# Performance work log

Measured on AMD Instinct MI355X. Metric: run time of the kernel, lower is better.

## Reference

```python
import jax, jax.numpy as jnp
import numpy as np

B, N, D = 2, 2048, 1024          # batch, seq (= wh*ww), model dim
H, HD = 16, 64                   # heads, head_dim (inner_dim = H*HD = D)
MLP = 4096                       # SwiGLU hidden dim
WSY, WSX = 16, 32                # ws_y = wh//2, ws_x = ww//2  (wh=32, ww=64)
EPS = float(jnp.finfo(jnp.float32).eps)  # torch RMSNorm default eps


def setup_inputs() -> dict:
    key = jax.random.key(0)
    ks = jax.random.split(key, 8)
    return {
        "x": jax.random.normal(ks[0], (B, N, D), jnp.float32),
        "t": jax.random.normal(ks[1], (B,), jnp.float32),
        "dt": jax.random.normal(ks[2], (B, D), jnp.float32),
        "w_qkv": (jax.random.normal(ks[3], (3 * H * HD, D), jnp.float32) * 0.02),
        "w_o": (jax.random.normal(ks[4], (D, H * HD), jnp.float32) * 0.02),
        "w1": (jax.random.normal(ks[5], (2 * MLP, D), jnp.float32) * 0.02),
        "w2": (jax.random.normal(ks[6], (D, MLP), jnp.float32) * 0.02),
        "g_attn": jnp.ones((D,), jnp.float32),  # RMSNorm weight (attn)
        "g_ff": jnp.ones((D,), jnp.float32),    # RMSNorm weight (ffn)
    }


def _rms(x, g):
    return x * jax.lax.rsqrt(jnp.mean(x * x, axis=-1, keepdims=True) + EPS) * g


def _win(x):
    # 'b h (wc_y wc_x ws_y ws_x) d' -> 'b h (wc_y ws_y wc_x ws_x) d'
    b, h, n, d = x.shape
    return x.reshape(b, h, 2, 2, WSY, WSX, d).transpose(0, 1, 2, 4, 3, 5, 6).reshape(b, h, n, d)


def _unwin(x):
    # inverse of _win
    b, h, n, d = x.shape
    return x.reshape(b, h, 2, WSY, 2, WSX, d).transpose(0, 1, 2, 4, 3, 5, 6).reshape(b, h, n, d)


def reference(x, t, dt, w_qkv, w_o, w1, w2, g_attn, g_ff):
    # ---- SPAttention (pre-norm); all-to-all is identity on 1 device ----
    h = _rms(x, g_attn)
    qkv = h @ w_qkv.T                              # [B,N,3*H*HD]
    q, k, v = jnp.split(qkv, 3, axis=-1)
    as_heads = lambda z: z.reshape(B, N, H, HD).transpose(0, 2, 1, 3)  # b h n d
    q, k, v = _win(as_heads(q)), _win(as_heads(k)), _win(as_heads(v))
    # NOTE: the source computes RoPE2D(q), RoPE2D(k) but discards the result;
    # attention consumes the UNROTATED seq_gathered_q/k/v. Faithful: no rotation.
    scale = 1.0 / jnp.sqrt(jnp.float32(HD))        # SDPA default scale
    s = jnp.einsum('bhqd,bhkd->bhqk', q, k) * scale
    a = jax.nn.softmax(s, axis=-1)
    o = jnp.einsum('bhqk,bhkd->bhqd', a, v)
    o = _unwin(o).transpose(0, 2, 1, 3).reshape(B, N, H * HD)
    x = x + o @ w_o.T                               # residual
    # ---- SwiGLU FeedForward (pre-norm) + residual ----
    hf = _rms(x, g_ff)
    gate, up = jnp.split(hf @ w1.T, 2, axis=-1)
    return x + (jax.nn.silu(gate) * up) @ w2.T
```

## Files before the change

### kernel.cpp

```cpp
#include <hip/hip_runtime.h>
#include <cstdint>
#include <cstddef>

typedef __attribute__((ext_vector_type(8)))  __bf16 bf16x8;
typedef __attribute__((ext_vector_type(4)))  __bf16 bf16x4;
typedef __attribute__((ext_vector_type(4)))  float  f32x4;
typedef __attribute__((ext_vector_type(16))) float  f32x16;
typedef __attribute__((ext_vector_type(2)))  uint32_t u32x2;
typedef __attribute__((ext_vector_type(4)))  uint32_t u32x4;

#define MFMA_BF16(a, b, c) __builtin_amdgcn_mfma_f32_16x16x32_bf16((a), (b), (c), 0, 0, 0)
#define MFMA32(a, b, c)    __builtin_amdgcn_mfma_f32_32x32x16_bf16((a), (b), (c), 0, 0, 0)

__device__ __forceinline__ void gload_lds16(const __bf16* src, __bf16* lds_dst) {
    __builtin_amdgcn_global_load_lds(
        (const __attribute__((address_space(1))) void*)(const_cast<__bf16*>(src)),
        (__attribute__((address_space(3))) void*)(lds_dst), 16, 0, 0);
}

__device__ __forceinline__ uint32_t pack2(float a, float b) {
    uint16_t ua = __builtin_bit_cast(uint16_t, (__bf16)a);
    uint16_t ub = __builtin_bit_cast(uint16_t, (__bf16)b);
    return (uint32_t)ua | ((uint32_t)ub << 16);
}

__device__ __forceinline__ int xcd_swz(int lid, int n) {
    return (lid & 7) * (n >> 3) + (lid >> 3);
}

__global__ __launch_bounds__(256) void cvt4_kernel(const float* __restrict__ s0,
                                                   const float* __restrict__ s1,
                                                   const float* __restrict__ s2,
                                                   const float* __restrict__ s3,
                                                   __bf16* __restrict__ d0,
                                                   __bf16* __restrict__ d1,
                                                   __bf16* __restrict__ d2,
                                                   __bf16* __restrict__ d3) {
    int b = blockIdx.x;
    const float* s; __bf16* d; int off;
    if (b < 3072)       { s = s0; d = d0; off = b; }
    else if (b < 4096)  { s = s1; d = d1; off = b - 3072; }
    else if (b < 12288) { s = s2; d = d2; off = b - 4096; }
    else                { s = s3; d = d3; off = b - 12288; }
    int i = off * 256 + threadIdx.x;
    float4 v = reinterpret_cast<const float4*>(s)[i];
    bf16x4 o;
    o[0] = (__bf16)v.x; o[1] = (__bf16)v.y; o[2] = (__bf16)v.z; o[3] = (__bf16)v.w;
    reinterpret_cast<bf16x4*>(d)[i] = o;
}

__global__ __launch_bounds__(256) void rmsnorm_kernel(const float* __restrict__ x,
                                                      const float* __restrict__ g,
                                                      __bf16* __restrict__ out) {
    const int row = blockIdx.x;
    const int t = threadIdx.x;
    float4 v = reinterpret_cast<const float4*>(x + (size_t)row * 1024)[t];
    float ss = v.x * v.x + v.y * v.y + v.z * v.z + v.w * v.w;
#pragma unroll
    for (int m = 1; m < 64; m <<= 1) ss += __shfl_xor(ss, m);
    __shared__ float sred[4];
    if ((t & 63) == 0) sred[t >> 6] = ss;
    __syncthreads();
    float tot = sred[0] + sred[1] + sred[2] + sred[3];
    float rs = rsqrtf(tot * (1.0f / 1024.0f) + 1.1920928955078125e-07f);
    float4 gv = reinterpret_cast<const float4*>(g)[t];
    bf16x4 o;
    o[0] = (__bf16)(v.x * rs * gv.x);
    o[1] = (__bf16)(v.y * rs * gv.y);
    o[2] = (__bf16)(v.z * rs * gv.z);
    o[3] = (__bf16)(v.w * rs * gv.w);
    *reinterpret_cast<bf16x4*>(out + (size_t)row * 1024 + t * 4) = o;
}

__global__ __launch_bounds__(256) void rmsnorm_b_kernel(const __bf16* __restrict__ x,
                                                        const float* __restrict__ g,
                                                        __bf16* __restrict__ out) {
    const int row = blockIdx.x;
    const int t = threadIdx.x;
    bf16x4 v4 = reinterpret_cast<const bf16x4*>(x + (size_t)row * 1024)[t];
    float a = (float)v4[0], b = (float)v4[1], c = (float)v4[2], d = (float)v4[3];
    float ss = a * a + b * b + c * c + d * d;
#pragma unroll
    for (int m = 1; m < 64; m <<= 1) ss += __shfl_xor(ss, m);
    __shared__ float sred[4];
    if ((t & 63) == 0) sred[t >> 6] = ss;
    __syncthreads();
    float tot = sred[0] + sred[1] + sred[2] + sred[3];
    float rs = rsqrtf(tot * (1.0f / 1024.0f) + 1.1920928955078125e-07f);
    float4 gv = reinterpret_cast<const float4*>(g)[t];
    bf16x4 o;
    o[0] = (__bf16)(a * rs * gv.x);
    o[1] = (__bf16)(b * rs * gv.y);
    o[2] = (__bf16)(c * rs * gv.z);
    o[3] = (__bf16)(d * rs * gv.w);
    *reinterpret_cast<bf16x4*>(out + (size_t)row * 1024 + t * 4) = o;
}

template <int MODE, int NB, int SQ>
__global__ __launch_bounds__(256) void gemm_nt(const __bf16* __restrict__ A, int lda,
                                               const __bf16* __restrict__ B, int ldb,
                                               __bf16* __restrict__ outb,
                                               float* __restrict__ outf,
                                               const float* __restrict__ resid,
                                               const __bf16* __restrict__ residb,
                                               __bf16* __restrict__ vt,
                                               int K, int ldo) {
    constexpr int BN = NB * 32;
    __shared__ __attribute__((aligned(16))) __bf16 As[128 * 64];
    __shared__ __attribute__((aligned(16))) __bf16 Bs[BN * 64];
    const int t = threadIdx.x;
    const int lane = t & 63;
    const int wid = t >> 6;
    int bm, bn;
    if (SQ) {
        int lid = blockIdx.x + blockIdx.y * gridDim.x;
        int c = lid & 7, i = lid >> 3;
        bm = (c & 1) * 16 + (i & 15);
        bn = (c >> 1) * 16 + (i >> 4);
    } else {
        int nwg = gridDim.x * gridDim.y;
        int sid = xcd_swz(blockIdx.x + blockIdx.y * gridDim.x, nwg);
        bm = sid % gridDim.x; bn = sid / gridDim.x;
    }
    const int wm = (wid >> 1) * 64, wn = (wid & 1) * (NB * 16);
    f32x4 acc[4][NB] = {};

    for (int kt = 0; kt < K; kt += 64) {
        __syncthreads();
#pragma unroll
        for (int i = 0; i < 4; ++i) {
            int L = i * 256 + t;
            int r = L >> 3, s = L & 7;
            int c = s ^ (r & 7);
            gload_lds16(A + (size_t)(bm * 128 + r) * lda + kt + c * 8, As + L * 8);
        }
#pragma unroll
        for (int i = 0; i < NB; ++i) {
            int L = i * 256 + t;
            int r = L >> 3, s = L & 7;
            int c = s ^ (r & 7);
            int rb = bn * BN + r;
            int srow = (MODE == 2) ? ((rb >> 1) + ((rb & 1) << 12)) : rb;
            gload_lds16(B + (size_t)srow * ldb + kt + c * 8, Bs + L * 8);
        }
        __syncthreads();
#pragma unroll
        for (int ks = 0; ks < 2; ++ks) {
            bf16x8 af[4], bfr[NB];
#pragma unroll
            for (int mi = 0; mi < 4; ++mi) {
                int r = wm + mi * 16 + (lane & 15);
                int slot = (ks * 4 + (lane >> 4)) ^ (r & 7);
                af[mi] = *reinterpret_cast<const bf16x8*>(As + r * 64 + slot * 8);
            }
#pragma unroll
            for (int ni = 0; ni < NB; ++ni) {
                int r = wn + ni * 16 + (lane & 15);
                int slot = (ks * 4 + (lane >> 4)) ^ (r & 7);
                bfr[ni] = *reinterpret_cast<const bf16x8*>(Bs + r * 64 + slot * 8);
            }
            __builtin_amdgcn_s_setprio(1);
#pragma unroll
            for (int mi = 0; mi < 4; ++mi)
#pragma unroll
                for (int ni = 0; ni < NB; ++ni)
                    acc[mi][ni] = MFMA_BF16(af[mi], bfr[ni], acc[mi][ni]);
            __builtin_amdgcn_s_setprio(0);
        }
    }
    const int row0 = bm * 128 + wm + ((lane >> 4) << 2);
    const int col0 = bn * BN + wn + (lane & 15);
    if (MODE == 4 && bn >= 16) {
#pragma unroll
        for (int mi = 0; mi < 4; ++mi)
#pragma unroll
            for (int ni = 0; ni < NB; ++ni) {
                bf16x4 o4;
#pragma unroll
                for (int r2 = 0; r2 < 4; ++r2) o4[r2] = (__bf16)acc[mi][ni][r2];
                int n0 = row0 + mi * 16;
                int bb = n0 >> 11, nn = n0 & 2047;
                int vc = col0 + ni * 16 - 2048;
                *reinterpret_cast<bf16x4*>(
                    vt + ((size_t)(bb * 16 + (vc >> 6)) * 64 + (vc & 63)) * 2048 + nn) = o4;
            }
        return;
    }
#pragma unroll
    for (int mi = 0; mi < 4; ++mi)
#pragma unroll
        for (int ni = 0; ni < NB; ++ni)
#pragma unroll
            for (int r2 = 0; r2 < 4; ++r2) {
                int row = row0 + mi * 16 + r2;
                int col = col0 + ni * 16;
                float v = acc[mi][ni][r2];
                size_t idx = (size_t)row * ldo + col;
                if (MODE == 0 || MODE == 4) {
                    outb[idx] = (__bf16)v;
                } else if (MODE == 1) {
                    outb[idx] = (__bf16)(v + resid[idx]);
                } else if (MODE == 3) {
                    outf[idx] = v + (float)residb[idx];
                } else {
                    float pv = __shfl_xor(v, 1);
                    if (!(lane & 1)) {
                        float sg = v / (1.0f + __expf(-v));
                        outb[(size_t)row * ldo + (col >> 1)] = (__bf16)(sg * pv);
                    }
                }
            }
}

__global__ __launch_bounds__(256) void attn_kernel(const __bf16* __restrict__ qkv,
                                                   const __bf16* __restrict__ vt,
                                                   float* __restrict__ opart,
                                                   float* __restrict__ lpart) {
    __shared__ __attribute__((aligned(16))) __bf16 Ks[128 * 64];
    __shared__ __attribute__((aligned(16))) __bf16 Vs[64 * 128];
    const int t = threadIdx.x;
    const int lane = t & 63;
    const int w = t >> 6;
    const int hi = lane >> 5;
    const int l31 = lane & 31;
    const int nwg = gridDim.x * gridDim.y;
    const int sid = xcd_swz(blockIdx.x + blockIdx.y * gridDim.x, nwg);
    const int qb = sid % gridDim.x;
    const int bh = sid / gridDim.x;
    const int kz = blockIdx.z;
    const int b = bh >> 4, h = bh & 15;
    const __bf16* qp = qkv + (size_t)b * 2048 * 3072 + h * 64;
    const __bf16* kp = qp + 1024;
    const __bf16* vtp = vt + (size_t)bh * 64 * 2048;
    const int q0 = qb * 128 + w * 32;

    const float SC = 0.18033688011112042f;
    bf16x8 qf[4];
#pragma unroll
    for (int s = 0; s < 4; ++s) {
        bf16x8 raw = *reinterpret_cast<const bf16x8*>(
            qp + (size_t)(q0 + l31) * 3072 + s * 16 + hi * 8);
        bf16x8 sc;
#pragma unroll
        for (int j = 0; j < 8; ++j) sc[j] = (__bf16)((float)raw[j] * SC);
        qf[s] = sc;
    }

    f32x16 oa[2] = {};
    float l_run = 0.0f;

    auto stage = [&](int kt) {
#pragma unroll
        for (int i = 0; i < 4; ++i) {
            int L = i * 256 + t;
            int r = L >> 3, s = L & 7;
            int c = s ^ (r & 7);
            gload_lds16(kp + (size_t)(kt + r) * 3072 + c * 8, &Ks[L * 8]);
        }
#pragma unroll
        for (int i = 0; i < 4; ++i) {
            int L = i * 256 + t;
            int r = L >> 4, s = L & 15;
            int c = s ^ (r & 15);
            gload_lds16(vtp + (size_t)r * 2048 + kt + c * 8, &Vs[L * 8]);
        }
    };

    const int kt0 = kz * 1024;
    for (int kt = kt0; kt < kt0 + 1024; kt += 128) {
        stage(kt);
        asm volatile("s_waitcnt vmcnt(0)\n\ts_barrier" ::: "memory");

#pragma unroll
        for (int h2 = 0; h2 < 2; ++h2) {
            f32x16 st[2];
#pragma unroll
            for (int r = 0; r < 16; ++r) { st[0][r] = -6.0f; st[1][r] = -6.0f; }
            __builtin_amdgcn_s_setprio(1);
#pragma unroll
            for (int s = 0; s < 4; ++s) {
#pragma unroll
                for (int mb = 0; mb < 2; ++mb) {
                    int r = h2 * 64 + mb * 32 + l31;
                    int sl = (s * 2 + hi) ^ (r & 7);
                    bf16x8 kf = *reinterpret_cast<const bf16x8*>(&Ks[r * 64 + sl * 8]);
                    st[mb] = MFMA32(kf, qf[s], st[mb]);
                }
            }
            __builtin_amdgcn_s_setprio(0);

            float ps = 0.0f;
#pragma unroll
            for (int mb = 0; mb < 2; ++mb)
#pragma unroll
                for (int r = 0; r < 16; ++r) {
                    float p = exp2f(st[mb][r]);
                    st[mb][r] = p;
                    ps += p;
                }
            ps += __shfl_xor(ps, 32);
            l_run += ps;

            uint32_t pk[16];
#pragma unroll
            for (int mb = 0; mb < 2; ++mb)
#pragma unroll
                for (int i2 = 0; i2 < 8; ++i2)
                    pk[mb * 8 + i2] = pack2(st[mb][2 * i2], st[mb][2 * i2 + 1]);

            __builtin_amdgcn_s_setprio(1);
#pragma unroll
            for (int s2 = 0; s2 < 4; ++s2) {
                const int I0 = (s2 >> 1) * 8 + (s2 & 1) * 4;
                u32x2 w02 = __builtin_amdgcn_permlane32_swap(pk[I0], pk[I0 + 2], false, false);
                u32x2 w13 = __builtin_amdgcn_permlane32_swap(pk[I0 + 1], pk[I0 + 3], false, false);
                u32x4 fv;
                fv[0] = w02[0]; fv[1] = w13[0]; fv[2] = w02[1]; fv[3] = w13[1];
                bf16x8 pa = __builtin_bit_cast(bf16x8, fv);
#pragma unroll
                for (int nb = 0; nb < 2; ++nb) {
                    int rv = nb * 32 + l31;
                    int ch = h2 * 8 + s2 * 2 + hi;
                    int sl = ch ^ (rv & 15);
                    bf16x8 vf = *reinterpret_cast<const bf16x8*>(&Vs[rv * 128 + sl * 8]);
                    oa[nb] = MFMA32(pa, vf, oa[nb]);
                }
            }
            __builtin_amdgcn_s_setprio(0);
        }
        __syncthreads();
    }

#pragma unroll
    for (int r = 0; r < 16; ++r) {
        int crow = (r & 3) + 8 * (r >> 2) + 4 * hi;
        int row = q0 + crow;
        size_t base = (size_t)kz * 4194304 + ((size_t)b * 2048 + row) * 1024 + h * 64 + l31;
        opart[base]      = oa[0][r];
        opart[base + 32] = oa[1][r];
    }
    if (hi == 0)
        lpart[kz * 65536 + bh * 2048 + q0 + l31] = l_run;
}

__global__ __launch_bounds__(256) void attn_comb(const float* __restrict__ op,
                                                 const float* __restrict__ lp,
                                                 __bf16* __restrict__ o) {
    const int row = blockIdx.x;
    const int t = threadIdx.x;
    const int b = row >> 11, q = row & 2047;
    const int c0 = t * 4;
    const int h = c0 >> 6;
    const int li = (b * 16 + h) * 2048 + q;
    float l = lp[li] + lp[65536 + li];
    float inv = 1.0f / l;
    float4 p0 = *reinterpret_cast<const float4*>(op + (size_t)row * 1024 + c0);
    float4 p1 = *reinterpret_cast<const float4*>(op + 4194304 + (size_t)row * 1024 + c0);
    bf16x4 o4;
    o4[0] = (__bf16)((p0.x + p1.x) * inv);
    o4[1] = (__bf16)((p0.y + p1.y) * inv);
    o4[2] = (__bf16)((p0.z + p1.z) * inv);
    o4[3] = (__bf16)((p0.w + p1.w) * inv);
    *reinterpret_cast<bf16x4*>(o + (size_t)row * 1024 + c0) = o4;
}

extern "C" void kernel_launch(void* const* d_in, const int* in_sizes, int n_in,
                              void* d_out, int out_size, void* d_ws, size_t ws_size,
                              hipStream_t stream) {
    const float* x      = (const float*)d_in[0];
    const float* w_qkv  = (const float*)d_in[3];
    const float* w_o    = (const float*)d_in[4];
    const float* w1     = (const float*)d_in[5];
    const float* w2     = (const float*)d_in[6];
    const float* g_attn = (const float*)d_in[7];
    const float* g_ff   = (const float*)d_in[8];
    float* out = (float*)d_out;

    char* ws = (char*)d_ws;
    size_t off = 0;
    auto alloc = [&](size_t bytes) -> void* {
        void* p = ws + off;
        off += (bytes + 255) & ~(size_t)255;
        return p;
    };
    __bf16* wqkv_b = (__bf16*)alloc((size_t)3072 * 1024 * 2);
    __bf16* wo_b   = (__bf16*)alloc((size_t)1024 * 1024 * 2);
    __bf16* w1_b   = (__bf16*)alloc((size_t)8192 * 1024 * 2);
    __bf16* w2_b   = (__bf16*)alloc((size_t)1024 * 4096 * 2);
    __bf16* h_b    = (__bf16*)alloc((size_t)4096 * 1024 * 2);
    __bf16* qkv_b  = (__bf16*)alloc((size_t)4096 * 3072 * 2);
    __bf16* o_b    = (__bf16*)alloc((size_t)4096 * 1024 * 2);
    __bf16* x2b    = (__bf16*)alloc((size_t)4096 * 1024 * 2);
    __bf16* vt_b   = (__bf16*)alloc((size_t)32 * 64 * 2048 * 2);
    float*  opart  = (float*)alloc((size_t)2 * 4096 * 1024 * 4);
    float*  lpart  = (float*)alloc((size_t)2 * 32 * 2048 * 4);
    __bf16* act_b  = qkv_b;

    cvt4_kernel<<<16384, 256, 0, stream>>>(w_qkv, w_o, w1, w2,
                                           wqkv_b, wo_b, w1_b, w2_b);

    rmsnorm_kernel<<<4096, 256, 0, stream>>>(x, g_attn, h_b);
    gemm_nt<4, 4, 0><<<dim3(32, 24), 256, 0, stream>>>(h_b, 1024, wqkv_b, 1024,
                                                       qkv_b, nullptr, nullptr, nullptr,
                                                       vt_b, 1024, 3072);
    attn_kernel<<<dim3(16, 32, 2), 256, 0, stream>>>(qkv_b, vt_b, opart, lpart);
    attn_comb<<<4096, 256, 0, stream>>>(opart, lpart, o_b);
    gemm_nt<1, 2, 0><<<dim3(32, 16), 256, 0, stream>>>(o_b, 1024, wo_b, 1024,
                                                       x2b, nullptr, x, nullptr,
                                                       nullptr, 1024, 1024);
    rmsnorm_b_kernel<<<4096, 256, 0, stream>>>(x2b, g_ff, h_b);
    gemm_nt<2, 4, 1><<<dim3(32, 64), 256, 0, stream>>>(h_b, 1024, w1_b, 1024,
                                                       act_b, nullptr, nullptr, nullptr,
                                                       nullptr, 1024, 4096);
    gemm_nt<3, 2, 0><<<dim3(32, 16), 256, 0, stream>>>(act_b, 4096, w2_b, 4096,
                                                       nullptr, out, nullptr, x2b,
                                                       nullptr, 4096, 1024);
}
```

Before: 308.6 us.

## Switch GEMM inner loop to 32x32x16 MFMA with precomputed load offsets

Replaces the 16x16x32 bf16 MFMA tiles in the shared GEMM kernel with 32x32x16 MFMA, so each wave covers its tile with fewer, larger matrix instructions and fewer LDS fragment reads per FLOP. Global-load source pointers and swizzled LDS read offsets are now computed once before the K loop instead of on every iteration. The epilogues are rewritten for the 32x32 accumulator layout. This raises accumulator register pressure and changes the LDS access pattern, which could affect occupancy or bank conflicts.

Result: no change. 312.8 us (+1.4%).

```diff
diff --git a/kernel.cpp b/kernel.cpp
--- a/kernel.cpp
+++ b/kernel.cpp
@@ -9,8 +9,7 @@
 typedef __attribute__((ext_vector_type(2)))  uint32_t u32x2;
 typedef __attribute__((ext_vector_type(4)))  uint32_t u32x4;
 
-#define MFMA_BF16(a, b, c) __builtin_amdgcn_mfma_f32_16x16x32_bf16((a), (b), (c), 0, 0, 0)
-#define MFMA32(a, b, c)    __builtin_amdgcn_mfma_f32_32x32x16_bf16((a), (b), (c), 0, 0, 0)
+#define MFMA32(a, b, c) __builtin_amdgcn_mfma_f32_32x32x16_bf16((a), (b), (c), 0, 0, 0)
 
 __device__ __forceinline__ void gload_lds16(const __bf16* src, __bf16* lds_dst) {
     __builtin_amdgcn_global_load_lds(
@@ -96,7 +95,7 @@
     *reinterpret_cast<bf16x4*>(out + (size_t)row * 1024 + t * 4) = o;
 }
 
-template <int MODE, int NB, int SQ>
+template <int MODE, int BN32, int SQ>
 __global__ __launch_bounds__(256) void gemm_nt(const __bf16* __restrict__ A, int lda,
                                                const __bf16* __restrict__ B, int ldb,
                                                __bf16* __restrict__ outb,
@@ -105,12 +104,15 @@
                                                const __bf16* __restrict__ residb,
                                                __bf16* __restrict__ vt,
                                                int K, int ldo) {
-    constexpr int BN = NB * 32;
+    constexpr int BN = BN32 * 32;
+    constexpr int NBW = BN32 / 2;
     __shared__ __attribute__((aligned(16))) __bf16 As[128 * 64];
     __shared__ __attribute__((aligned(16))) __bf16 Bs[BN * 64];
     const int t = threadIdx.x;
     const int lane = t & 63;
     const int wid = t >> 6;
+    const int hi = lane >> 5;
+    const int l31 = lane & 31;
     int bm, bn;
     if (SQ) {
         int lid = blockIdx.x + blockIdx.y * gridDim.x;
@@ -122,79 +124,102 @@
         int sid = xcd_swz(blockIdx.x + blockIdx.y * gridDim.x, nwg);
         bm = sid % gridDim.x; bn = sid / gridDim.x;
     }
-    const int wm = (wid >> 1) * 64, wn = (wid & 1) * (NB * 16);
-    f32x4 acc[4][NB] = {};
+    const int wm = (wid >> 1) * 64, wn = (wid & 1) * (BN / 2);
+
+    const __bf16* pa[4];
+    const __bf16* pb[BN32];
+#pragma unroll
+    for (int i = 0; i < 4; ++i) {
+        int L = i * 256 + t, r = L >> 3, c = (L & 7) ^ (r & 7);
+        pa[i] = A + (size_t)(bm * 128 + r) * lda + c * 8;
+    }
+#pragma unroll
+    for (int i = 0; i < BN32; ++i) {
+        int L = i * 256 + t, r = L >> 3, c = (L & 7) ^ (r & 7);
+        int rb = bn * BN + r;
+        int srow = (MODE == 2) ? ((rb >> 1) + ((rb & 1) << 12)) : rb;
+        pb[i] = B + (size_t)srow * ldb + c * 8;
+    }
+
+    uint32_t aoff[2][4], boff[NBW][4];
+#pragma unroll
+    for (int mi = 0; mi < 2; ++mi) {
+        int r = wm + mi * 32 + l31;
+#pragma unroll
+        for (int kk = 0; kk < 4; ++kk)
+            aoff[mi][kk] = r * 64 + (((kk * 2 + hi) ^ (r & 7)) * 8);
+    }
+#pragma unroll
+    for (int ni = 0; ni < NBW; ++ni) {
+        int r = wn + ni * 32 + l31;
+#pragma unroll
+        for (int kk = 0; kk < 4; ++kk)
+            boff[ni][kk] = r * 64 + (((kk * 2 + hi) ^ (r & 7)) * 8);
+    }
+
+    f32x16 acc[2][NBW] = {};
 
     for (int kt = 0; kt < K; kt += 64) {
         __syncthreads();
 #pragma unroll
         for (int i = 0; i < 4; ++i) {
-            int L = i * 256 + t;
-            int r = L >> 3, s = L & 7;
-            int c = s ^ (r & 7);
-            gload_lds16(A + (size_t)(bm * 128 + r) * lda + kt + c * 8, As + L * 8);
-        }
-#pragma unroll
-        for (int i = 0; i < NB; ++i) {
-            int L = i * 256 + t;
-            int r = L >> 3, s = L & 7;
-            int c = s ^ (r & 7);
-            int rb = bn * BN + r;
-            int srow = (MODE == 2) ? ((rb >> 1) + ((rb & 1) << 12)) : rb;
-            gload_lds16(B + (size_t)srow * ldb + kt + c * 8, Bs + L * 8);
+            gload_lds16(pa[i], As + (i * 256 + t) * 8);
+            pa[i] += 64;
+        }
+#pragma unroll
+        for (int i = 0; i < BN32; ++i) {
+            gload_lds16(pb[i], Bs + (i * 256 + t) * 8);
+            pb[i] += 64;
         }
         __syncthreads();
 #pragma unroll
-        for (int ks = 0; ks < 2; ++ks) {
-            bf16x8 af[4], bfr[NB];
-#pragma unroll
-            for (int mi = 0; mi < 4; ++mi) {
-                int r = wm + mi * 16 + (lane & 15);
-                int slot = (ks * 4 + (lane >> 4)) ^ (r & 7);
-                af[mi] = *reinterpret_cast<const bf16x8*>(As + r * 64 + slot * 8);
-            }
-#pragma unroll
-            for (int ni = 0; ni < NB; ++ni) {
-                int r = wn + ni * 16 + (lane & 15);
-                int slot = (ks * 4 + (lane >> 4)) ^ (r & 7);
-                bfr[ni] = *reinterpret_cast<const bf16x8*>(Bs + r * 64 + slot * 8);
-            }
+        for (int kk = 0; kk < 4; ++kk) {
+            bf16x8 af[2], bfr[NBW];
+#pragma unroll
+            for (int mi = 0; mi < 2; ++mi)
+                af[mi] = *reinterpret_cast<const bf16x8*>(As + aoff[mi][kk]);
+#pragma unroll
+            for (int ni = 0; ni < NBW; ++ni)
+                bfr[ni] = *reinterpret_cast<const bf16x8*>(Bs + boff[ni][kk]);
             __builtin_amdgcn_s_setprio(1);
 #pragma unroll
-            for (int mi = 0; mi < 4; ++mi)
-#pragma unroll
-                for (int ni = 0; ni < NB; ++ni)
-                    acc[mi][ni] = MFMA_BF16(af[mi], bfr[ni], acc[mi][ni]);
+            for (int mi = 0; mi < 2; ++mi)
+#pragma unroll
+                for (int ni = 0; ni < NBW; ++ni)
+                    acc[mi][ni] = MFMA32(af[mi], bfr[ni], acc[mi][ni]);
             __builtin_amdgcn_s_setprio(0);
         }
     }
-    const int row0 = bm * 128 + wm + ((lane >> 4) << 2);
-    const int col0 = bn * BN + wn + (lane & 15);
+
+    const int row0 = bm * 128 + wm + 4 * hi;
+    const int col0 = bn * BN + wn + l31;
     if (MODE == 4 && bn >= 16) {
 #pragma unroll
-        for (int mi = 0; mi < 4; ++mi)
-#pragma unroll
-            for (int ni = 0; ni < NB; ++ni) {
-                bf16x4 o4;
-#pragma unroll
-                for (int r2 = 0; r2 < 4; ++r2) o4[r2] = (__bf16)acc[mi][ni][r2];
-                int n0 = row0 + mi * 16;
-                int bb = n0 >> 11, nn = n0 & 2047;
-                int vc = col0 + ni * 16 - 2048;
-                *reinterpret_cast<bf16x4*>(
-                    vt + ((size_t)(bb * 16 + (vc >> 6)) * 64 + (vc & 63)) * 2048 + nn) = o4;
-            }
+        for (int mi = 0; mi < 2; ++mi)
+#pragma unroll
+            for (int ni = 0; ni < NBW; ++ni)
+#pragma unroll
+                for (int g = 0; g < 4; ++g) {
+                    bf16x4 o4;
+#pragma unroll
+                    for (int j = 0; j < 4; ++j) o4[j] = (__bf16)acc[mi][ni][g * 4 + j];
+                    int n0 = row0 + mi * 32 + 8 * g;
+                    int bb = n0 >> 11, nn = n0 & 2047;
+                    int vc = col0 + ni * 32 - 2048;
+                    *reinterpret_cast<bf16x4*>(
+                        vt + ((size_t)(bb * 16 + (vc >> 6)) * 64 + (vc & 63)) * 2048 + nn) = o4;
+                }
         return;
     }
 #pragma unroll
-    for (int mi = 0; mi < 4; ++mi)
-#pragma unroll
-        for (int ni = 0; ni < NB; ++ni)
-#pragma unroll
-            for (int r2 = 0; r2 < 4; ++r2) {
-                int row = row0 + mi * 16 + r2;
-                int col = col0 + ni * 16;
-                float v = acc[mi][ni][r2];
+    for (int mi = 0; mi < 2; ++mi)
+#pragma unroll
+        for (int ni = 0; ni < NBW; ++ni)
+#pragma unroll
+            for (int r = 0; r < 16; ++r) {
+                int row = row0 + mi * 32 + (r & 3) + 8 * (r >> 2);
+                int col = col0 + ni * 32;
+                float v = acc[mi][ni][r];
                 size_t idx = (size_t)row * ldo + col;
                 if (MODE == 0 || MODE == 4) {
                     outb[idx] = (__bf16)v;
```
